# Performance work log

Measured on AMD Instinct MI355X. Metric: run time of the kernel, lower is better.

The kernel has to match this reference:

```python
import jax, jax.numpy as jnp
import numpy as np

# dims
B, P, H, W = 4, 512, 32, 32
C2 = P // 2            # 256 per-branch channels
HEAD = 4
DH = C2 // HEAD        # 64 head dim
L = H * W              # 1024 tokens
DI = 2 * C2            # 512 mamba d_inner (expand=2)
N = 64                 # d_state
R = (C2 + 15) // 16    # 16 dt_rank
KC = 4                 # d_conv


def setup_inputs() -> dict:
    key = jax.random.key(0)
    ks = jax.random.split(key, 32)
    f32 = jnp.float32
    def nrm(k, shape, s=0.02):
        return jax.random.normal(k, shape, f32) * s
    inp = {}
    inp['x'] = jax.random.normal(ks[0], (B, P, H, W), f32)
    # GambaCell rel-pos + gate conv
    inp['rel_h_c'] = jax.random.normal(ks[1], (1, C2, 1, H), f32)
    inp['rel_w_c'] = jax.random.normal(ks[2], (1, C2, W, 1), f32)
    inp['gate_w'] = nrm(ks[3], (C2, C2, 3))
    inp['gate_b'] = jnp.zeros((C2,), f32)
    # Mamba params
    inp['W_in'] = nrm(ks[4], (2 * DI, C2))
    inp['conv_w'] = nrm(ks[5], (DI, KC), 0.2)
    inp['conv_b'] = jnp.zeros((DI,), f32)
    inp['W_x'] = nrm(ks[6], (R + 2 * N, DI))
    inp['W_dt'] = nrm(ks[7], (DI, R), 0.1)
    inp['b_dt'] = jnp.full((DI,), -4.0, f32)
    inp['A_log'] = jnp.broadcast_to(jnp.log(jnp.arange(1, N + 1, dtype=f32)), (DI, N)).copy()
    inp['D_p'] = jnp.ones((DI,), f32)
    inp['W_out'] = nrm(ks[8], (C2, DI))
    # MHSA params (1x1 convs -> dense)
    inp['Wq'] = nrm(ks[9], (C2, C2)); inp['bq'] = jnp.zeros((C2,), f32)
    inp['Wk'] = nrm(ks[10], (C2, C2)); inp['bk'] = jnp.zeros((C2,), f32)
    inp['Wv'] = nrm(ks[11], (C2, C2)); inp['bv'] = jnp.zeros((C2,), f32)
    inp['rel_h_m'] = jax.random.normal(ks[12], (1, HEAD, DH, 1, H), f32) * 0.02
    inp['rel_w_m'] = jax.random.normal(ks[13], (1, HEAD, DH, W, 1), f32) * 0.02
    inp['reg_qk'] = jax.random.normal(ks[14], (1, L, L), f32)
    inp['reg_v'] = jax.random.normal(ks[15], (1, DH, L), f32)
    # Gating params
    inp['Wa'] = nrm(ks[16], (P, C2)); inp['ba'] = jnp.zeros((P,), f32)
    inp['Wb'] = nrm(ks[17], (P, C2)); inp['bb'] = jnp.zeros((P,), f32)
    inp['Wg'] = nrm(ks[18], (1, P)); inp['bg'] = jnp.zeros((1,), f32)
    return inp


def _silu(t):
    return t * jax.nn.sigmoid(t)


def _conv1x1(w, b, t):  # Conv2d kernel_size=1
    return jnp.einsum('oc,bchw->bohw', w, t) + b[None, :, None, None]


def _mamba(seq, W_in, conv_w, conv_b, W_x, W_dt, b_dt, A_log, D_p, W_out):
    # seq: (B, L, C2)
    Bn = seq.shape[0]
    xz = seq @ W_in.T                       # (B,L,2*DI)
    xi, z = jnp.split(xz, 2, axis=-1)
    # causal depthwise conv1d, kernel 4, left-pad 3, trimmed to L
    xc = jnp.transpose(xi, (0, 2, 1))       # (B,DI,L)
    xp = jnp.pad(xc, ((0, 0), (0, 0), (KC - 1, 0)))
    conv = conv_b[None, :, None]
    for kk in range(KC):
        conv = conv + conv_w[None, :, kk, None] * xp[:, :, kk:kk + L]
    xs = _silu(conv).transpose(0, 2, 1)     # (B,L,DI)
    x_dbl = xs @ W_x.T                      # (B,L,R+2N)
    dt = jax.nn.softplus(x_dbl[..., :R] @ W_dt.T + b_dt)   # (B,L,DI)
    Bm = x_dbl[..., R:R + N]                # (B,L,N)
    Cm = x_dbl[..., R + N:]                 # (B,L,N)
    A = -jnp.exp(A_log)                     # (DI,N)

    def step(h, t):
        dt_t, B_t, C_t, u_t = t             # (B,DI),(B,N),(B,N),(B,DI)
        dA = jnp.exp(dt_t[..., None] * A)   # (B,DI,N)
        h = dA * h + (dt_t * u_t)[..., None] * B_t[:, None, :]
        y = jnp.sum(h * C_t[:, None, :], axis=-1)
        return h, y

    h0 = jnp.zeros((Bn, DI, N), seq.dtype)
    scan_in = (dt.transpose(1, 0, 2), Bm.transpose(1, 0, 2),
               Cm.transpose(1, 0, 2), xs.transpose(1, 0, 2))
    _, ys = jax.lax.scan(step, h0, scan_in)  # (L,B,DI)
    y = ys.transpose(1, 0, 2) + D_p * xs
    y = y * _silu(z)
    return y @ W_out.T                      # (B,L,C2)


def _forward(x, rel_h_c, rel_w_c, gate_w, gate_b, W_in, conv_w, conv_b, W_x,
             W_dt, b_dt, A_log, D_p, W_out, Wq, bq, Wk, bk, Wv, bv,
             rel_h_m, rel_w_m, reg_qk, reg_v, Wa, ba, Wb, bb, Wg, bg):
    Bn = x.shape[0]
    x1, x2 = x[:, :C2], x[:, C2:]
    # --- GambaCell branch ---
    seq = x1.reshape(Bn, C2, L).transpose(0, 2, 1)          # (B,L,C2)
    pos = (rel_h_c + rel_w_c).reshape(1, C2, L).transpose(0, 2, 1)
    seq = seq + pos
    sc = seq.transpose(0, 2, 1)                             # (B,C2,L)
    ctx = jax.nn.sigmoid(
        jax.lax.conv_general_dilated(sc, gate_w, (1,), [(1, 1)],
                                     dimension_numbers=('NCH', 'OIH', 'NCH'))
        + gate_b[None, :, None]).transpose(0, 2, 1)          # (B,L,C2)
    ym = _mamba(seq, W_in, conv_w, conv_b, W_x, W_dt, b_dt, A_log, D_p, W_out)
    # faithful to original: view (B,L,C)->(B,C,H,W) with no permute
    out1 = (ym * ctx).reshape(Bn, C2, H, W)
    # --- MHSA branch ---
    q = _conv1x1(Wq, bq, x2).reshape(Bn, HEAD, DH, L)
    k = _conv1x1(Wk, bk, x2).reshape(Bn, HEAD, DH, L)
    v = _conv1x1(Wv, bv, x2).reshape(Bn, HEAD, DH, L)
    cc = jnp.einsum('bhdi,bhdj->bhij', q, k)                # content-content
    posm = (rel_h_m + rel_w_m).reshape(HEAD, DH, L)
    cp = jnp.einsum('hdi,bhdj->bhij', posm, q)              # position^T @ q
    energy = cc + cp                                         # (B,HEAD,L,L)
    e = jnp.concatenate([energy, jnp.broadcast_to(reg_qk[None], (Bn, 1, L, L))], axis=1)
    vp = jnp.concatenate([v, jnp.broadcast_to(reg_v[None], (Bn, 1, DH, L))], axis=1)
    attn = jax.nn.softmax(e, axis=-1)
    out = jnp.einsum('bndj,bnij->bndi', vp, attn)           # v @ attn^T
    out2 = out[:, :HEAD].reshape(Bn, C2, H, W)
    # --- Gating fusion ---
    a_proj = _conv1x1(Wa, ba, out1)
    b_proj = _conv1x1(Wb, bb, out2)
    ga = jax.nn.sigmoid(_conv1x1(Wg, bg, a_proj))
    gb = jax.nn.sigmoid(_conv1x1(Wg, bg, b_proj))
    return ga * a_proj + gb * b_proj                        # (B,P,H,W)


def reference(x, rel_h_c, rel_w_c, gate_w, gate_b, W_in, conv_w, conv_b, W_x,
              W_dt, b_dt, A_log, D_p, W_out, Wq, bq, Wk, bk, Wv, bv,
              rel_h_m, rel_w_m, reg_qk, reg_v, Wa, ba, Wb, bb, Wg, bg):
    return _forward(x, rel_h_c, rel_w_c, gate_w, gate_b, W_in, conv_w, conv_b,
                    W_x, W_dt, b_dt, A_log, D_p, W_out, Wq, bq, Wk, bk, Wv, bv,
                    rel_h_m, rel_w_m, reg_qk, reg_v, Wa, ba, Wb, bb, Wg, bg)
```

## Files before the change

### kernel.cpp

```cpp
#include <hip/hip_runtime.h>
#include <math.h>

static constexpr int Bn = 4, Pp = 512, C2 = 256, HEAD = 4, DHd = 64;
static constexpr int Ll = 1024, DIi = 512, Nn = 64, Rr = 16, KCc = 4;
static constexpr int XDW = 192;

#define DEVI __device__ __forceinline__

DEVI float sigf(float x){ return 1.0f/(1.0f+__expf(-x)); }
DEVI float softplusf(float x){ return x > 20.f ? x : log1pf(__expf(x)); }

DEVI unsigned short bfh(float f){
  unsigned int u = __float_as_uint(f);
  return (unsigned short)((u + 0x7FFFu + ((u>>16)&1u)) >> 16);
}
DEVI float bff(unsigned short h){ return __uint_as_float(((unsigned int)h)<<16); }

typedef __attribute__((ext_vector_type(8))) short  bf8v;
typedef __attribute__((ext_vector_type(4))) float  f4v;
typedef __attribute__((ext_vector_type(8))) unsigned short u16x8;

__global__ void k_transpose(const float* __restrict__ x, const float* __restrict__ rh,
                            const float* __restrict__ rw, float* __restrict__ seq,
                            float* __restrict__ x2seq){
  __shared__ float t[32][33];
  int b = blockIdx.z, c0 = blockIdx.y*32, l0 = blockIdx.x*32;
  for (int i = threadIdx.y; i < 32; i += 8)
    t[i][threadIdx.x] = x[((size_t)(b*Pp + c0 + i)*Ll) + l0 + threadIdx.x];
  __syncthreads();
  for (int i = threadIdx.y; i < 32; i += 8){
    int l = l0 + i, c = c0 + threadIdx.x;
    float v = t[threadIdx.x][i];
    if (c < C2){
      float pos = rh[c*32 + (l & 31)] + rw[c*32 + (l >> 5)];
      seq[(size_t)(b*Ll + l)*C2 + c] = v + pos;
    } else {
      x2seq[(size_t)(b*Ll + l)*C2 + (c - C2)] = v;
    }
  }
}

__global__ void __launch_bounds__(256) k_mgemmb(
    const float* __restrict__ A, const float* __restrict__ B,
    float* __restrict__ C, const float* __restrict__ bias,
    int M, int N, int K, int lda, int ldb, int ldc,
    long sA1, long sA2, long sB1, long sB2, long sC1, long sC2, int act)
{
  __shared__ __align__(16) unsigned short Ah[64*40], Al[64*40], Bh[64*40], Bl[64*40];
  int z = blockIdx.z;
  const float* Ab = A + (size_t)((z>>2)*sA1 + (z&3)*sA2);
  const float* Bb = B + (size_t)((z>>2)*sB1 + (z&3)*sB2);
  float*       Cb = C + (size_t)((z>>2)*sC1 + (z&3)*sC2);
  int m0 = blockIdx.y*64, n0 = blockIdx.x*64;
  int t = threadIdx.x;
  int w = t >> 6, l = t & 63;
  int g = l >> 4, r = l & 15;
  int row0 = w*16;

  f4v acc[4];
  #pragma unroll
  for (int j=0;j<4;++j) acc[j] = (f4v){0.f,0.f,0.f,0.f};

  int sr = t >> 2;
  int sc = (t & 3) * 8;

  for (int k0 = 0; k0 < K; k0 += 32){
    {
      const float* src = Ab + (size_t)(m0+sr)*lda + k0 + sc;
      float4 v0 = *(const float4*)(src);
      float4 v1 = *(const float4*)(src+4);
      float f[8] = {v0.x,v0.y,v0.z,v0.w,v1.x,v1.y,v1.z,v1.w};
      u16x8 hv, lv;
      #pragma unroll
      for (int i=0;i<8;++i){
        unsigned short h = bfh(f[i]); hv[i] = h;
        lv[i] = bfh(f[i] - bff(h));
      }
      *(u16x8*)&Ah[sr*40+sc] = hv;
      *(u16x8*)&Al[sr*40+sc] = lv;
    }
    {
      const float* src = Bb + (size_t)(n0+sr)*ldb + k0 + sc;
      float4 v0 = *(const float4*)(src);
      float4 v1 = *(const float4*)(src+4);
      float f[8] = {v0.x,v0.y,v0.z,v0.w,v1.x,v1.y,v1.z,v1.w};
      u16x8 hv, lv;
      #pragma unroll
      for (int i=0;i<8;++i){
        unsigned short h = bfh(f[i]); hv[i] = h;
        lv[i] = bfh(f[i] - bff(h));
      }
      *(u16x8*)&Bh[sr*40+sc] = hv;
      *(u16x8*)&Bl[sr*40+sc] = lv;
    }
    __syncthreads();
    bf8v a_h = *(const bf8v*)&Ah[(row0+r)*40 + g*8];
    bf8v a_l = *(const bf8v*)&Al[(row0+r)*40 + g*8];
    #pragma unroll
    for (int j=0;j<4;++j){
      bf8v b_h = *(const bf8v*)&Bh[(j*16+r)*40 + g*8];
      bf8v b_l = *(const bf8v*)&Bl[(j*16+r)*40 + g*8];
      acc[j] = __builtin_amdgcn_mfma_f32_16x16x32_bf16(a_h, b_h, acc[j], 0, 0, 0);
      acc[j] = __builtin_amdgcn_mfma_f32_16x16x32_bf16(a_h, b_l, acc[j], 0, 0, 0);
      acc[j] = __builtin_amdgcn_mfma_f32_16x16x32_bf16(a_l, b_h, acc[j], 0, 0, 0);
    }
    __syncthreads();
  }
  #pragma unroll
  for (int j=0;j<4;++j){
    int n = n0 + j*16 + r;
    float bv = bias ? bias[n] : 0.f;
    #pragma unroll
    for (int q=0;q<4;++q){
      int m = m0 + row0 + g*4 + q;
      float v = acc[j][q] + bv;
      if (act == 1) v = sigf(v);
      Cb[(size_t)m*ldc + n] = v;
    }
  }
}

__global__ void __launch_bounds__(256) k_m128(
    const float* __restrict__ A, const float* __restrict__ B,
    float* __restrict__ C, const float* __restrict__ bias,
    int M, int N, int K, int lda, int ldb, int ldc,
    long sA1, long sA2, long sB1, long sB2, long sC1, long sC2, int act)
{
  __shared__ __align__(16) unsigned short Ah[128*40], Al[128*40], Bh[128*40], Bl[128*40];
  int z = blockIdx.z;
  const float* Ab = A + (size_t)((z>>2)*sA1 + (z&3)*sA2);
  const float* Bb = B + (size_t)((z>>2)*sB1 + (z&3)*sB2);
  float*       Cb = C + (size_t)((z>>2)*sC1 + (z&3)*sC2);
  int m0 = blockIdx.y*128, n0 = blockIdx.x*128;
  int t = threadIdx.x;
  int w = t >> 6, l = t & 63;
  int g = l >> 4, r = l & 15;
  int row0 = w*32;

  f4v acc[2][8];
  #pragma unroll
  for (int i=0;i<2;++i)
    #pragma unroll
    for (int j=0;j<8;++j) acc[i][j] = (f4v){0.f,0.f,0.f,0.f};

  int sr = t >> 1;
  int sc = (t & 1) * 16;

  for (int k0 = 0; k0 < K; k0 += 32){
    {
      const float* src = Ab + (size_t)(m0+sr)*lda + k0 + sc;
      float4 v0 = *(const float4*)(src);
      float4 v1 = *(const float4*)(src+4);
      float4 v2 = *(const float4*)(src+8);
      float4 v3 = *(const float4*)(src+12);
      float f[16] = {v0.x,v0.y,v0.z,v0.w,v1.x,v1.y,v1.z,v1.w,
                     v2.x,v2.y,v2.z,v2.w,v3.x,v3.y,v3.z,v3.w};
      u16x8 hv0, lv0, hv1, lv1;
      #pragma unroll
      for (int i=0;i<8;++i){
        unsigned short h = bfh(f[i]); hv0[i] = h;
        lv0[i] = bfh(f[i] - bff(h));
      }
      #pragma unroll
      for (int i=0;i<8;++i){
        unsigned short h = bfh(f[8+i]); hv1[i] = h;
        lv1[i] = bfh(f[8+i] - bff(h));
      }
      *(u16x8*)&Ah[sr*40+sc]   = hv0;  *(u16x8*)&Ah[sr*40+sc+8] = hv1;
      *(u16x8*)&Al[sr*40+sc]   = lv0;  *(u16x8*)&Al[sr*40+sc+8] = lv1;
    }
    {
      const float* src = Bb + (size_t)(n0+sr)*ldb + k0 + sc;
      float4 v0 = *(const float4*)(src);
      float4 v1 = *(const float4*)(src+4);
      float4 v2 = *(const float4*)(src+8);
      float4 v3 = *(const float4*)(src+12);
      float f[16] = {v0.x,v0.y,v0.z,v0.w,v1.x,v1.y,v1.z,v1.w,
                     v2.x,v2.y,v2.z,v2.w,v3.x,v3.y,v3.z,v3.w};
      u16x8 hv0, lv0, hv1, lv1;
      #pragma unroll
      for (int i=0;i<8;++i){
        unsigned short h = bfh(f[i]); hv0[i] = h;
        lv0[i] = bfh(f[i] - bff(h));
      }
      #pragma unroll
      for (int i=0;i<8;++i){
        unsigned short h = bfh(f[8+i]); hv1[i] = h;
        lv1[i] = bfh(f[8+i] - bff(h));
      }
      *(u16x8*)&Bh[sr*40+sc]   = hv0;  *(u16x8*)&Bh[sr*40+sc+8] = hv1;
      *(u16x8*)&Bl[sr*40+sc]   = lv0;  *(u16x8*)&Bl[sr*40+sc+8] = lv1;
    }
    __syncthreads();
    bf8v a_h0 = *(const bf8v*)&Ah[(row0+r)*40 + g*8];
    bf8v a_l0 = *(const bf8v*)&Al[(row0+r)*40 + g*8];
    bf8v a_h1 = *(const bf8v*)&Ah[(row0+16+r)*40 + g*8];
    bf8v a_l1 = *(const bf8v*)&Al[(row0+16+r)*40 + g*8];
    #pragma unroll
    for (int j=0;j<8;++j){
      bf8v b_h = *(const bf8v*)&Bh[(j*16+r)*40 + g*8];
      bf8v b_l = *(const bf8v*)&Bl[(j*16+r)*40 + g*8];
      acc[0][j] = __builtin_amdgcn_mfma_f32_16x16x32_bf16(a_h0, b_h, acc[0][j], 0, 0, 0);
      acc[0][j] = __builtin_amdgcn_mfma_f32_16x16x32_bf16(a_h0, b_l, acc[0][j], 0, 0, 0);
      acc[0][j] = __builtin_amdgcn_mfma_f32_16x16x32_bf16(a_l0, b_h, acc[0][j], 0, 0, 0);
      acc[1][j] = __builtin_amdgcn_mfma_f32_16x16x32_bf16(a_h1, b_h, acc[1][j], 0, 0, 0);
      acc[1][j] = __builtin_amdgcn_mfma_f32_16x16x32_bf16(a_h1, b_l, acc[1][j], 0, 0, 0);
      acc[1][j] = __builtin_amdgcn_mfma_f32_16x16x32_bf16(a_l1, b_h, acc[1][j], 0, 0, 0);
    }
    __syncthreads();
  }
  #pragma unroll
  for (int i=0;i<2;++i){
    #pragma unroll
    for (int j=0;j<8;++j){
      int n = n0 + j*16 + r;
      float bv = bias ? bias[n] : 0.f;
      #pragma unroll
      for (int q=0;q<4;++q){
        int m = m0 + row0 + i*16 + g*4 + q;
        float v = acc[i][j][q] + bv;
        if (act == 1) v = sigf(v);
        Cb[(size_t)m*ldc + n] = v;
      }
    }
  }
}

__global__ void k_padwx(const float* __restrict__ W_x, float* __restrict__ W_xp){
  int idx = blockIdx.x*256 + threadIdx.x;
  int row = idx >> 9;
  W_xp[idx] = (row < 144) ? W_x[(size_t)(row)*512 + (idx & 511)] : 0.f;
}

__global__ void k_im2col(const float* __restrict__ seq, float* __restrict__ A2){
  int idx = blockIdx.x*256 + threadIdx.x;
  int j  = idx % 768;
  int bl = idx / 768;
  int kk = j >> 8, c = j & 255;
  int l = bl & 1023, b = bl >> 10;
  int ls = l + kk - 1;
  float v = 0.f;
  if (ls >= 0 && ls < Ll) v = seq[(size_t)(b*Ll + ls)*C2 + c];
  A2[idx] = v;
}

__global__ void k_packw(const float* __restrict__ gw, float* __restrict__ W2){
  int idx = blockIdx.x*256 + threadIdx.x;
  int j = idx % 768, o = idx / 768;
  int kk = j >> 8, i = j & 255;
  W2[idx] = gw[(size_t)(o*256 + i)*3 + kk];
}

__global__ void k_dwconv(const float* __restrict__ xz, const float* __restrict__ cw,
                         const float* __restrict__ cb, float* __restrict__ xs){
  int idx = blockIdx.x*256 + threadIdx.x;
  int d = idx & 511; int bl = idx >> 9; int l = bl & 1023; int b = bl >> 10;
  float s = cb[d];
  #pragma unroll
  for (int kk = 0; kk < 4; ++kk){
    int ls = l - 3 + kk;
    if (ls >= 0) s = fmaf(cw[d*4+kk], xz[(size_t)(b*Ll+ls)*1024 + d], s);
  }
  xs[idx] = s * sigf(s);
}

__global__ void k_pret(const float* __restrict__ xdbl, const float* __restrict__ xs,
                       const float* __restrict__ W_dt, const float* __restrict__ b_dt,
                       float* __restrict__ dtT, float* __restrict__ dtuT){
  __shared__ float X[32][17];
  __shared__ float Wd[32][17];
  __shared__ float xsb[32][33];
  int b = blockIdx.z, d0 = blockIdx.y*32, l0 = blockIdx.x*32;
  int tx = threadIdx.x, ty = threadIdx.y;
  for (int i = ty; i < 32; i += 8){
    if (tx < 16)      X[i][tx]      = xdbl[(size_t)(b*Ll + l0 + i)*XDW + tx];
    else              Wd[i][tx-16]  = W_dt[(size_t)(d0 + i)*16 + tx - 16];
    xsb[i][tx] = xs[(size_t)(b*Ll + l0 + i)*512 + d0 + tx];
  }
  __syncthreads();
  for (int dy = ty; dy < 32; dy += 8){
    int d = d0 + dy;
    float v = b_dt[d];
    #pragma unroll
    for (int r = 0; r < 16; ++r) v = fmaf(Wd[dy][r], X[tx][r], v);
    float dt = softplusf(v);
    size_t o = ((size_t)(b*512 + d))*Ll + l0 + tx;
    dtT[o]  = dt;
    dtuT[o] = dt * xsb[tx][dy];
  }
}

__global__ void __launch_bounds__(256, 1) k_scan6(
    const float* __restrict__ dtT, const float* __restrict__ dtuT,
    const float* __restrict__ xdbl, const float* __restrict__ A_log,
    float* __restrict__ yT){
  __shared__ float Bs[32*64];
  __shared__ float Cs[32*64];
  __shared__ float pb[4*32*65];
  int t = threadIdx.x;
  int w = t >> 6, lane = t & 63;
  int blk = blockIdx.x;
  int b = blk >> 7, grp = blk & 127;
  int d = grp*4 + w;
  float Ac = -__expf(A_log[d*64 + lane]);
  float h = 0.f;
  size_t base = (size_t)b*Ll;
  size_t bd   = ((size_t)(b*512 + d))*Ll;
  int jl = lane & 31;
  bool lo = lane < 32;
  float* pbw = &pb[w*2080];
  for (int c0 = 0; c0 < Ll; c0 += 32){
    float dtv = 0.f, duv = 0.f;
    if (lo){
      dtv = dtT[bd + c0 + lane];
      duv = dtuT[bd + c0 + lane];
    }
    #pragma unroll
    for (int kk = 0; kk < 8; ++kk){
      int i = t + kk*256;
      int row = i >> 6, col = i & 63;
      size_t r2 = (base + c0 + row)*XDW;
      Bs[i] = xdbl[r2 + 16 + col];
      Cs[i] = xdbl[r2 + 80 + col];
    }
    __syncthreads();
    float ev[32], gv[32];
    #pragma unroll
    for (int l = 0; l < 32; ++l){
      float sdt = __shfl(dtv, l);
      float sdu = __shfl(duv, l);
      ev[l] = __expf(sdt*Ac);
      gv[l] = sdu*Bs[l*64 + lane];
    }
    #pragma unroll
    for (int l = 0; l < 32; ++l){
      h = fmaf(ev[l], h, gv[l]);
      pbw[l*65 + lane] = h*Cs[l*64 + lane];
    }
    __syncthreads();
    {
      const float* rp = &pbw[jl*65 + (lo ? 0 : 32)];
      float s0=0.f, s1=0.f, s2=0.f, s3=0.f;
      #pragma unroll
      for (int n = 0; n < 32; n += 4){
        s0 += rp[n]; s1 += rp[n+1]; s2 += rp[n+2]; s3 += rp[n+3];
      }
      float p = (s0+s1)+(s2+s3);
      p += __shfl_xor(p, 32);
      if (lo) yT[bd + c0 + jl] = p;
    }
    __syncthreads();
  }
}

__global__ void k_ytrans(const float* __restrict__ yT, const float* __restrict__ xs,
                         const float* __restrict__ xz, const float* __restrict__ D_p,
                         float* __restrict__ y){
  __shared__ float t[32][33];
  int b = blockIdx.z, d0 = blockIdx.y*32, l0 = blockIdx.x*32;
  int tx = threadIdx.x, ty = threadIdx.y;
  for (int i = ty; i < 32; i += 8)
    t[i][tx] = yT[((size_t)(b*512 + d0 + i))*Ll + l0 + tx];
  __syncthreads();
  for (int i = ty; i < 32; i += 8){
    int d = d0 + tx;
    size_t bl = (size_t)b*Ll + l0 + i;
    float p  = t[tx][i];
    float u  = xs[bl*512 + d];
    float zv = xz[bl*1024 + 512 + d];
    y[bl*512 + d] = (p + D_p[d]*u) * (zv * sigf(zv));
  }
}

__global__ void k_pack_ab(const float* __restrict__ qt, const float* __restrict__ kt,
                          const float* __restrict__ rhm, const float* __restrict__ rwm,
                          float* __restrict__ Ab, float* __restrict__ Bb){
  int idx = blockIdx.x*256 + threadIdx.x;
  int dd = idx & 127;
  int i  = (idx >> 7) & 1023;
  int h  = (idx >> 17) & 3;
  int b  = idx >> 19;
  float av, bv;
  if (dd < 64){
    size_t q = (size_t)(b*Ll + i)*C2 + h*64 + dd;
    av = qt[q]; bv = kt[q];
  } else {
    int d = dd - 64;
    av = rhm[(h*64+d)*32 + (i & 31)] + rwm[(h*64+d)*32 + (i >> 5)];
    bv = qt[(size_t)(b*Ll + i)*C2 + h*64 + d];
  }
  Ab[idx] = av; Bb[idx] = bv;
}

__global__ void k_vtrans(const float* __restrict__ vt, float* __restrict__ vT){
  __shared__ float t[32][33];
  int b = blockIdx.z, c0 = blockIdx.y*32, j0 = blockIdx.x*32;
  for (int i = threadIdx.y; i < 32; i += 8)
    t[i][threadIdx.x] = vt[(size_t)(b*Ll + j0 + i)*C2 + c0 + threadIdx.x];
  __syncthreads();
  for (int i = threadIdx.y; i < 32; i += 8)
    vT[((size_t)(b*C2 + c0 + i))*Ll + j0 + threadIdx.x] = t[threadIdx.x][i];
}

__global__ void __launch_bounds__(256) k_softmax(float* __restrict__ e){
  __shared__ float red[4];
  __shared__ float red2[4];
  size_t row = blockIdx.x;
  float* p = e + row*1024;
  int t = threadIdx.x;
  float v0 = p[t], v1 = p[t+256], v2 = p[t+512], v3 = p[t+768];
  float mx = fmaxf(fmaxf(v0,v1), fmaxf(v2,v3));
  #pragma unroll
  for (int off=32; off; off>>=1) mx = fmaxf(mx, __shfl_xor(mx, off));
  if ((t&63)==0) red[t>>6] = mx;
  __syncthreads();
  mx = fmaxf(fmaxf(red[0],red[1]), fmaxf(red[2],red[3]));
  v0 = __expf(v0-mx); v1 = __expf(v1-mx); v2 = __expf(v2-mx); v3 = __expf(v3-mx);
  float s = v0+v1+v2+v3;
  #pragma unroll
  for (int off=32; off; off>>=1) s += __shfl_xor(s, off);
  if ((t&63)==0) red2[t>>6] = s;
  __syncthreads();
  s = red2[0]+red2[1]+red2[2]+red2[3];
  float inv = 1.0f/s;
  p[t] = v0*inv; p[t+256] = v1*inv; p[t+512] = v2*inv; p[t+768] = v3*inv;
}

__global__ void k_mulshuf(const float* __restrict__ ym, const float* __restrict__ ctx,
                          float* __restrict__ out1t){
  __shared__ float t[32][33];
  int b = blockIdx.z >> 2, s1 = blockIdx.z & 3;
  int c0 = blockIdx.y*32, s00 = blockIdx.x*32;
  for (int i = threadIdx.y; i < 32; i += 8){
    int c = c0 + i;
    int l = c*4 + s1;
    size_t off = ((size_t)(b*Ll + l))*C2 + s00 + threadIdx.x;
    t[i][threadIdx.x] = ym[off] * ctx[off];
  }
  __syncthreads();
  for (int i = threadIdx.y; i < 32; i += 8){
    int s0 = s00 + i, c = c0 + threadIdx.x;
    int s = s1*256 + s0;
    out1t[((size_t)(b*Ll + s))*C2 + c] = t[threadIdx.x][i];
  }
}

__global__ void __launch_bounds__(256) k_gates(
    const float* __restrict__ ap, const float* __restrict__ bp,
    const float* __restrict__ Wg, const float* __restrict__ bg, float* __restrict__ g){
  __shared__ float ra[4], rb[4];
  int bl = blockIdx.x; int t = threadIdx.x;
  float sa = 0.f, sb = 0.f;
  const float* a = ap + (size_t)bl*512;
  const float* bq = bp + (size_t)bl*512;
  for (int pp = t; pp < 512; pp += 256){ float w = Wg[pp]; sa = fmaf(w, a[pp], sa); sb = fmaf(w, bq[pp], sb); }
  #pragma unroll
  for (int off=32; off; off>>=1){ sa += __shfl_xor(sa,off); sb += __shfl_xor(sb,off); }
  if ((t&63)==0){ ra[t>>6]=sa; rb[t>>6]=sb; }
  __syncthreads();
  if (t==0){
    float b0 = bg[0];
    g[bl]        = sigf(ra[0]+ra[1]+ra[2]+ra[3] + b0);
    g[4096 + bl] = sigf(rb[0]+rb[1]+rb[2]+rb[3] + b0);
  }
}

__global__ void k_final(const float* __restrict__ ap, const float* __restrict__ bp,
                        const float* __restrict__ g, float* __restrict__ out){
  int bpid = blockIdx.x; int b = bpid >> 9, p = bpid & 511;
  for (int l = threadIdx.x; l < Ll; l += 256){
    int bl = b*Ll + l;
    float ga = g[bl], gb = g[4096 + bl];
    out[((size_t)(b*Pp + p) << 10) + l] =
        ga*ap[(size_t)bl*512 + p] + gb*bp[(size_t)bl*512 + p];
  }
}

static inline void mgemm(hipStream_t s, const float* A, const float* B, float* C,
                         const float* bias, int M, int N, int K, int lda, int ldb, int ldc,
                         int act){
  dim3 g(N/64, M/64, 1), blk(256);
  k_mgemmb<<<g, blk, 0, s>>>(A,B,C,bias,M,N,K,lda,ldb,ldc, 0,0,0,0,0,0, act);
}

extern "C" void kernel_launch(void* const* d_in, const int* in_sizes, int n_in,
                              void* d_out, int out_size, void* d_ws, size_t ws_size,
                              hipStream_t stream) {
  const float* x      = (const float*)d_in[0];
  const float* rh_c   = (const float*)d_in[1];
  const float* rw_c   = (const float*)d_in[2];
  const float* gate_w = (const float*)d_in[3];
  const float* gate_b = (const float*)d_in[4];
  const float* W_in   = (const float*)d_in[5];
  const float* conv_w = (const float*)d_in[6];
  const float* conv_b = (const float*)d_in[7];
  const float* W_x    = (const float*)d_in[8];
  const float* W_dt   = (const float*)d_in[9];
  const float* b_dt   = (const float*)d_in[10];
  const float* A_log  = (const float*)d_in[11];
  const float* D_p    = (const float*)d_in[12];
  const float* W_out  = (const float*)d_in[13];
  const float* Wq     = (const float*)d_in[14];
  const float* bq     = (const float*)d_in[15];
  const float* Wk     = (const float*)d_in[16];
  const float* bk     = (const float*)d_in[17];
  const float* Wv     = (const float*)d_in[18];
  const float* bv     = (const float*)d_in[19];
  const float* rhm    = (const float*)d_in[20];
  const float* rwm    = (const float*)d_in[21];
  const float* Wa     = (const float*)d_in[24];
  const float* ba     = (const float*)d_in[25];
  const float* Wb     = (const float*)d_in[26];
  const float* bb     = (const float*)d_in[27];
  const float* Wg     = (const float*)d_in[28];
  const float* bg     = (const float*)d_in[29];
  float* out = (float*)d_out;
  float* ws  = (float*)d_ws;

  float* seq    = ws;
  float* x2seq  = ws +  1048576;
  float* qt     = ws +  2097152;
  float* kt     = ws +  3145728;
  float* vt     = ws +  4194304;
  float* Abuf   = ws +  5242880;
  float* Bbuf   = ws +  7340032;
  float* arena  = ws +  9437184;
  float* out2   = ws + 26214400;
  float* out1   = ws + 27262976;
  float* aproj  = ws + 28311552;
  float* bproj  = ws + 30408704;
  float* gates  = ws + 32505856;
  float* W2     = ws + 32514048;
  float* A2   = arena;
  float* ctx  = arena +  3145728;
  float* xz   = arena +  4194304;
  float* xs   = arena +  8388608;
  float* xdbl = arena + 10485760;
  float* yT   = arena + 11272192;
  float* yb   = arena + 13369344;
  float* ym   = arena + 15466496;
  float* energy = arena;
  float* vT   = aproj;
  float* dtT  = Abuf;
  float* dtuT = Bbuf;
  float* W_xp = qt;

  k_transpose<<<dim3(32,16,4), dim3(32,8), 0, stream>>>(x, rh_c, rw_c, seq, x2seq);

  mgemm(stream, x2seq, Wq, qt, bq, 4096,256,256, 256,256,256, 0);
  mgemm(stream, x2seq, Wk, kt, bk, 4096,256,256, 256,256,256, 0);
  mgemm(stream, x2seq, Wv, vt, bv, 4096,256,256, 256,256,256, 0);
  k_pack_ab<<<8192, 256, 0, stream>>>(qt, kt, rhm, rwm, Abuf, Bbuf);
  k_vtrans<<<dim3(32,8,4), dim3(32,8), 0, stream>>>(vt, vT);
  {
    dim3 g(8, 8, 16), blk(256);
    k_m128<<<g, blk, 0, stream>>>(Abuf, Bbuf, energy, nullptr,
        1024,1024,128, 128,128,1024,
        4L*131072, 131072, 4L*131072, 131072, 4L*1048576, 1048576, 0);
  }
  k_softmax<<<16384, 256, 0, stream>>>(energy);
  {
    dim3 g(1, 16, 16), blk(256);
    k_mgemmb<<<g, blk, 0, stream>>>(energy, vT, out2, nullptr,
        1024,64,1024, 1024,1024,256,
        4L*1048576, 1048576, 262144, 65536, 262144, 64, 0);
  }

  k_packw<<<768, 256, 0, stream>>>(gate_w, W2);
  k_padwx<<<384, 256, 0, stream>>>(W_x, W_xp);
  k_im2col<<<12288, 256, 0, stream>>>(seq, A2);
  mgemm(stream, A2, W2, ctx, gate_b, 4096,256,768, 768,768,256, 1);
  {
    dim3 g(8, 32, 1), blk(256);
    k_m128<<<g, blk, 0, stream>>>(seq, W_in, xz, nullptr,
        4096,1024,256, 256,256,1024, 0,0,0,0,0,0, 0);
  }
  k_dwconv<<<8192, 256, 0, stream>>>(xz, conv_w, conv_b, xs);
  mgemm(stream, xs, W_xp, xdbl, nullptr, 4096,192,512, 512,512,XDW, 0);
  k_pret<<<dim3(32,16,4), dim3(32,8), 0, stream>>>(xdbl, xs, W_dt, b_dt, dtT, dtuT);
  k_scan6<<<512, 256, 0, stream>>>(dtT, dtuT, xdbl, A_log, yT);
  k_ytrans<<<dim3(32,16,4), dim3(32,8), 0, stream>>>(yT, xs, xz, D_p, yb);
  mgemm(stream, yb, W_out, ym, nullptr, 4096,256,512, 512,512,256, 0);
  k_mulshuf<<<dim3(8,8,16), dim3(32,8), 0, stream>>>(ym, ctx, out1);

  mgemm(stream, out1, Wa, aproj, ba, 4096,512,256, 256,256,512, 0);
  mgemm(stream, out2, Wb, bproj, bb, 4096,512,256, 256,256,512, 0);
  k_gates<<<4096, 256, 0, stream>>>(aproj, bproj, Wg, bg, gates);
  k_final<<<2048, 256, 0, stream>>>(aproj, bproj, gates, out);
}
```

Measured before the change: 565.3 us.

## Pre-split GEMM operands into bf16 hi/lo planes in producer kernels

```diff
diff --git a/kernel.cpp b/kernel.cpp
--- a/kernel.cpp
+++ b/kernel.cpp
@@ -15,14 +15,26 @@
   return (unsigned short)((u + 0x7FFFu + ((u>>16)&1u)) >> 16);
 }
 DEVI float bff(unsigned short h){ return __uint_as_float(((unsigned int)h)<<16); }
+DEVI void wsplit(float v, unsigned short* __restrict__ h, unsigned short* __restrict__ l,
+                 size_t i){
+  unsigned short hh = bfh(v);
+  h[i] = hh; l[i] = bfh(v - bff(hh));
+}
 
 typedef __attribute__((ext_vector_type(8))) short  bf8v;
 typedef __attribute__((ext_vector_type(4))) float  f4v;
 typedef __attribute__((ext_vector_type(8))) unsigned short u16x8;
 
+__global__ void k_split(const float* __restrict__ src, unsigned short* __restrict__ h,
+                        unsigned short* __restrict__ l, int n){
+  int i = blockIdx.x*256 + threadIdx.x;
+  if (i < n) wsplit(src[i], h, l, i);
+}
+
 __global__ void k_transpose(const float* __restrict__ x, const float* __restrict__ rh,
                             const float* __restrict__ rw, float* __restrict__ seq,
-                            float* __restrict__ x2seq){
+                            unsigned short* __restrict__ sh, unsigned short* __restrict__ sl,
+                            unsigned short* __restrict__ x2h, unsigned short* __restrict__ x2l){
   __shared__ float t[32][33];
   int b = blockIdx.z, c0 = blockIdx.y*32, l0 = blockIdx.x*32;
   for (int i = threadIdx.y; i < 32; i += 8)
@@ -33,24 +45,31 @@
     float v = t[threadIdx.x][i];
     if (c < C2){
       float pos = rh[c*32 + (l & 31)] + rw[c*32 + (l >> 5)];
-      seq[(size_t)(b*Ll + l)*C2 + c] = v + pos;
+      float vv = v + pos;
+      size_t o = (size_t)(b*Ll + l)*C2 + c;
+      seq[o] = vv;
+      wsplit(vv, sh, sl, o);
     } else {
-      x2seq[(size_t)(b*Ll + l)*C2 + (c - C2)] = v;
-    }
-  }
-}
-
-__global__ void __launch_bounds__(256) k_mgemmb(
-    const float* __restrict__ A, const float* __restrict__ B,
+      size_t o = (size_t)(b*Ll + l)*C2 + (c - C2);
+      wsplit(v, x2h, x2l, o);
+    }
+  }
+}
+
+__global__ void __launch_bounds__(256) k_hgemm(
+    const unsigned short* __restrict__ Ahp, const unsigned short* __restrict__ Alp,
+    const unsigned short* __restrict__ Bhp, const unsigned short* __restrict__ Blp,
     float* __restrict__ C, const float* __restrict__ bias,
     int M, int N, int K, int lda, int ldb, int ldc,
     long sA1, long sA2, long sB1, long sB2, long sC1, long sC2, int act)
 {
   __shared__ __align__(16) unsigned short Ah[64*40], Al[64*40], Bh[64*40], Bl[64*40];
   int z = blockIdx.z;
-  const float* Ab = A + (size_t)((z>>2)*sA1 + (z&3)*sA2);
-  const float* Bb = B + (size_t)((z>>2)*sB1 + (z&3)*sB2);
-  float*       Cb = C + (size_t)((z>>2)*sC1 + (z&3)*sC2);
+  const unsigned short* Abh = Ahp + (size_t)((z>>2)*sA1 + (z&3)*sA2);
+  const unsigned short* Abl = Alp + (size_t)((z>>2)*sA1 + (z&3)*sA2);
+  const unsigned short* Bbh = Bhp + (size_t)((z>>2)*sB1 + (z&3)*sB2);
+  const unsigned short* Bbl = Blp + (size_t)((z>>2)*sB1 + (z&3)*sB2);
+  float* Cb = C + (size_t)((z>>2)*sC1 + (z&3)*sC2);
   int m0 = blockIdx.y*64, n0 = blockIdx.x*64;
   int t = threadIdx.x;
   int w = t >> 6, l = t & 63;
@@ -65,34 +84,12 @@
   int sc = (t & 3) * 8;
 
   for (int k0 = 0; k0 < K; k0 += 32){
-    {
-      const float* src = Ab + (size_t)(m0+sr)*lda + k0 + sc;
-      float4 v0 = *(const float4*)(src);
-      float4 v1 = *(const float4*)(src+4);
-      float f[8] = {v0.x,v0.y,v0.z,v0.w,v1.x,v1.y,v1.z,v1.w};
-      u16x8 hv, lv;
-      #pragma unroll
-      for (int i=0;i<8;++i){
-        unsigned short h = bfh(f[i]); hv[i] = h;
-        lv[i] = bfh(f[i] - bff(h));
-      }
-      *(u16x8*)&Ah[sr*40+sc] = hv;
-      *(u16x8*)&Al[sr*40+sc] = lv;
-    }
-    {
-      const float* src = Bb + (size_t)(n0+sr)*ldb + k0 + sc;
-      float4 v0 = *(const float4*)(src);
-      float4 v1 = *(const float4*)(src+4);
-      float f[8] = {v0.x,v0.y,v0.z,v0.w,v1.x,v1.y,v1.z,v1.w};
-      u16x8 hv, lv;
-      #pragma unroll
-      for (int i=0;i<8;++i){
-        unsigned short h = bfh(f[i]); hv[i] = h;
-        lv[i] = bfh(f[i] - bff(h));
-      }
-      *(u16x8*)&Bh[sr*40+sc] = hv;
-      *(u16x8*)&Bl[sr*40+sc] = lv;
-    }
+    size_t ao = (size_t)(m0+sr)*lda + k0 + sc;
+    size_t bo = (size_t)(n0+sr)*ldb + k0 + sc;
+    *(u16x8*)&Ah[sr*40+sc] = *(const u16x8*)&Abh[ao];
+    *(u16x8*)&Al[sr*40+sc] = *(const u16x8*)&Abl[ao];
+    *(u16x8*)&Bh[sr*40+sc] = *(const u16x8*)&Bbh[bo];
+    *(u16x8*)&Bl[sr*40+sc] = *(const u16x8*)&Bbl[bo];
     __syncthreads();
     bf8v a_h = *(const bf8v*)&Ah[(row0+r)*40 + g*8];
     bf8v a_l = *(const bf8v*)&Al[(row0+r)*40 + g*8];
@@ -120,17 +117,20 @@
   }
 }
 
-__global__ void __launch_bounds__(256) k_m128(
-    const float* __restrict__ A, const float* __restrict__ B,
+__global__ void __launch_bounds__(256) k_h128(
+    const unsigned short* __restrict__ Ahp, const unsigned short* __restrict__ Alp,
+    const unsigned short* __restrict__ Bhp, const unsigned short* __restrict__ Blp,
     float* __restrict__ C, const float* __restrict__ bias,
     int M, int N, int K, int lda, int ldb, int ldc,
     long sA1, long sA2, long sB1, long sB2, long sC1, long sC2, int act)
 {
   __shared__ __align__(16) unsigned short Ah[128*40], Al[128*40], Bh[128*40], Bl[128*40];
   int z = blockIdx.z;
-  const float* Ab = A + (size_t)((z>>2)*sA1 + (z&3)*sA2);
-  const float* Bb = B + (size_t)((z>>2)*sB1 + (z&3)*sB2);
-  float*       Cb = C + (size_t)((z>>2)*sC1 + (z&3)*sC2);
+  const unsigned short* Abh = Ahp + (size_t)((z>>2)*sA1 + (z&3)*sA2);
+  const unsigned short* Abl = Alp + (size_t)((z>>2)*sA1 + (z&3)*sA2);
+  const unsigned short* Bbh = Bhp + (size_t)((z>>2)*sB1 + (z&3)*sB2);
+  const unsigned short* Bbl = Blp + (size_t)((z>>2)*sB1 + (z&3)*sB2);
+  float* Cb = C + (size_t)((z>>2)*sC1 + (z&3)*sC2);
   int m0 = blockIdx.y*128, n0 = blockIdx.x*128;
   int t = threadIdx.x;
   int w = t >> 6, l = t & 63;
@@ -147,50 +147,16 @@
   int sc = (t & 1) * 16;
 
   for (int k0 = 0; k0 < K; k0 += 32){
-    {
-      const float* src = Ab + (size_t)(m0+sr)*lda + k0 + sc;
-      float4 v0 = *(const float4*)(src);
-      float4 v1 = *(const float4*)(src+4);
-      float4 v2 = *(const float4*)(src+8);
-      float4 v3 = *(const float4*)(src+12);
-      float f[16] = {v0.x,v0.y,v0.z,v0.w,v1.x,v1.y,v1.z,v1.w,
-                     v2.x,v2.y,v2.z,v2.w,v3.x,v3.y,v3.z,v3.w};
-      u16x8 hv0, lv0, hv1, lv1;
-      #pragma unroll
-      for (int i=0;i<8;++i){
-        unsigned short h = bfh(f[i]); hv0[i] = h;
-        lv0[i] = bfh(f[i] - bff(h));
-      }
-      #pragma unroll
-      for (int i=0;i<8;++i){
-        unsigned short h = bfh(f[8+i]); hv1[i] = h;
-        lv1[i] = bfh(f[8+i] - bff(h));
-      }
-      *(u16x8*)&Ah[sr*40+sc]   = hv0;  *(u16x8*)&Ah[sr*40+sc+8] = hv1;
-      *(u16x8*)&Al[sr*40+sc]   = lv0;  *(u16x8*)&Al[sr*40+sc+8] = lv1;
-    }
-    {
-      const float* src = Bb + (size_t)(n0+sr)*ldb + k0 + sc;
-      float4 v0 = *(const float4*)(src);
-      float4 v1 = *(const float4*)(src+4);
-      float4 v2 = *(const float4*)(src+8);
-      float4 v3 = *(const float4*)(src+12);
-      float f[16] = {v0.x,v0.y,v0.z,v0.w,v1.x,v1.y,v1.z,v1.w,
-                     v2.x,v2.y,v2.z,v2.w,v3.x,v3.y,v3.z,v3.w};
-      u16x8 hv0, lv0, hv1, lv1;
-      #pragma unroll
-      for (int i=0;i<8;++i){
-        unsigned short h = bfh(f[i]); hv0[i] = h;
-        lv0[i] = bfh(f[i] - bff(h));
-      }
-      #pragma unroll
-      for (int i=0;i<8;++i){
-        unsigned short h = bfh(f[8+i]); hv1[i] = h;
-        lv1[i] = bfh(f[8+i] - bff(h));
-      }
-      *(u16x8*)&Bh[sr*40+sc]   = hv0;  *(u16x8*)&Bh[sr*40+sc+8] = hv1;
-      *(u16x8*)&Bl[sr*40+sc]   = lv0;  *(u16x8*)&Bl[sr*40+sc+8] = lv1;
-    }
+    size_t ao = (size_t)(m0+sr)*lda + k0 + sc;
+    size_t bo = (size_t)(n0+sr)*ldb + k0 + sc;
+    *(u16x8*)&Ah[sr*40+sc]   = *(const u16x8*)&Abh[ao];
+    *(u16x8*)&Ah[sr*40+sc+8] = *(const u16x8*)&Abh[ao+8];
+    *(u16x8*)&Al[sr*40+sc]   = *(const u16x8*)&Abl[ao];
+    *(u16x8*)&Al[sr*40+sc+8] = *(const u16x8*)&Abl[ao+8];
+    *(u16x8*)&Bh[sr*40+sc]   = *(const u16x8*)&Bbh[bo];
+    *(u16x8*)&Bh[sr*40+sc+8] = *(const u16x8*)&Bbh[bo+8];
+    *(u16x8*)&Bl[sr*40+sc]   = *(const u16x8*)&Bbl[bo];
+    *(u16x8*)&Bl[sr*40+sc+8] = *(const u16x8*)&Bbl[bo+8];
     __syncthreads();
     bf8v a_h0 = *(const bf8v*)&Ah[(row0+r)*40 + g*8];
     bf8v a_l0 = *(const bf8v*)&Al[(row0+r)*40 + g*8];
@@ -226,42 +192,49 @@
   }
 }
 
-__global__ void k_padwx(const float* __restrict__ W_x, float* __restrict__ W_xp){
+__global__ void k_padwx(const float* __restrict__ W_x, unsigned short* __restrict__ h,
+                        unsigned short* __restrict__ l){
   int idx = blockIdx.x*256 + threadIdx.x;
   int row = idx >> 9;
-  W_xp[idx] = (row < 144) ? W_x[(size_t)(row)*512 + (idx & 511)] : 0.f;
-}
-
-__global__ void k_im2col(const float* __restrict__ seq, float* __restrict__ A2){
+  float v = (row < 144) ? W_x[(size_t)row*512 + (idx & 511)] : 0.f;
+  wsplit(v, h, l, idx);
+}
+
+__global__ void k_im2col(const float* __restrict__ seq, unsigned short* __restrict__ h,
+                         unsigned short* __restrict__ l){
   int idx = blockIdx.x*256 + threadIdx.x;
   int j  = idx % 768;
   int bl = idx / 768;
   int kk = j >> 8, c = j & 255;
-  int l = bl & 1023, b = bl >> 10;
-  int ls = l + kk - 1;
+  int ll = bl & 1023, b = bl >> 10;
+  int ls = ll + kk - 1;
   float v = 0.f;
   if (ls >= 0 && ls < Ll) v = seq[(size_t)(b*Ll + ls)*C2 + c];
-  A2[idx] = v;
-}
-
-__global__ void k_packw(const float* __restrict__ gw, float* __restrict__ W2){
+  wsplit(v, h, l, idx);
+}
+
+__global__ void k_packw(const float* __restrict__ gw, unsigned short* __restrict__ h,
+                        unsigned short* __restrict__ l){
   int idx = blockIdx.x*256 + threadIdx.x;
   int j = idx % 768, o = idx / 768;
   int kk = j >> 8, i = j & 255;
-  W2[idx] = gw[(size_t)(o*256 + i)*3 + kk];
+  wsplit(gw[(size_t)(o*256 + i)*3 + kk], h, l, idx);
 }
 
 __global__ void k_dwconv(const float* __restrict__ xz, const float* __restrict__ cw,
-                         const float* __restrict__ cb, float* __restrict__ xs){
+                         const float* __restrict__ cb, float* __restrict__ xs,
+                         unsigned short* __restrict__ h, unsigned short* __restrict__ l){
   int idx = blockIdx.x*256 + threadIdx.x;
-  int d = idx & 511; int bl = idx >> 9; int l = bl & 1023; int b = bl >> 10;
+  int d = idx & 511; int bl = idx >> 9; int ll = bl & 1023; int b = bl >> 10;
   float s = cb[d];
   #pragma unroll
   for (int kk = 0; kk < 4; ++kk){
-    int ls = l - 3 + kk;
+    int ls = ll - 3 + kk;
     if (ls >= 0) s = fmaf(cw[d*4+kk], xz[(size_t)(b*Ll+ls)*1024 + d], s);
   }
-  xs[idx] = s * sigf(s);
+  float v = s * sigf(s);
+  xs[idx] = v;
+  wsplit(v, h, l, idx);
 }
 
 __global__ void k_pret(const float* __restrict__ xdbl, const float* __restrict__ xs,
@@ -355,7 +328,7 @@
 
 __global__ void k_ytrans(const float* __restrict__ yT, const float* __restrict__ xs,
                          const float* __restrict__ xz, const float* __restrict__ D_p,
-                         float* __restrict__ y){
+                         unsigned short* __restrict__ h, unsigned short* __restrict__ l){
   __shared__ float t[32][33];
   int b = blockIdx.z, d0 = blockIdx.y*32, l0 = blockIdx.x*32;
   int tx = threadIdx.x, ty = threadIdx.y;
@@ -368,13 +341,15 @@
     float p  = t[tx][i];
     float u  = xs[bl*512 + d];
     float zv = xz[bl*1024 + 512 + d];
-    y[bl*512 + d] = (p + D_p[d]*u) * (zv * sigf(zv));
+    float v = (p + D_p[d]*u) * (zv * sigf(zv));
+    wsplit(v, h, l, bl*512 + d);
   }
 }
 
 __global__ void k_pack_ab(const float* __restrict__ qt, const float* __restrict__ kt,
                           const float* __restrict__ rhm, const float* __restrict__ rwm,
-                          float* __restrict__ Ab, float* __restrict__ Bb){
+                          unsigned short* __restrict__ Ahp, unsigned short* __restrict__ Alp,
+                          unsigned short* __restrict__ Bhp, unsigned short* __restrict__ Blp){
   int idx = blockIdx.x*256 + threadIdx.x;
   int dd = idx & 127;
   int i  = (idx >> 7) & 1023;
@@ -389,17 +364,21 @@
     av = rhm[(h*64+d)*32 + (i & 31)] + rwm[(h*64+d)*32 + (i >> 5)];
     bv = qt[(size_t)(b*Ll + i)*C2 + h*64 + d];
   }
-  Ab[idx] = av; Bb[idx] = bv;
-}
-
-__global__ void k_vtrans(const float* __restrict__ vt, float* __restrict__ vT){
+  wsplit(av, Ahp, Alp, idx);
+  wsplit(bv, Bhp, Blp, idx);
+}
+
+__global__ void k_vtrans(const float* __restrict__ vt, unsigned short* __restrict__ h,
+                         unsigned short* __restrict__ l){
   __shared__ float t[32][33];
   int b = blockIdx.z, c0 = blockIdx.y*32, j0 = blockIdx.x*32;
   for (int i = threadIdx.y; i < 32; i += 8)
     t[i][threadIdx.x] = vt[(size_t)(b*Ll + j0 + i)*C2 + c0 + threadIdx.x];
   __syncthreads();
-  for (int i = threadIdx.y; i < 32; i += 8)
-    vT[((size_t)(b*C2 + c0 + i))*Ll + j0 + threadIdx.x] = t[threadIdx.x][i];
+  for (int i = threadIdx.y; i < 32; i += 8){
+    size_t o = ((size_t)(b*C2 + c0 + i))*Ll + j0 + threadIdx.x;
+    wsplit(t[threadIdx.x][i], h, l, o);
+  }
 }
 
 __global__ void __launch_bounds__(256) k_softmax(float* __restrict__ e){
@@ -423,25 +402,31 @@
   __syncthreads();
   s = red2[0]+red2[1]+red2[2]+red2[3];
   float inv = 1.0f/s;
-  p[t] = v0*inv; p[t+256] = v1*inv; p[t+512] = v2*inv; p[t+768] = v3*inv;
+  unsigned short* ph = (unsigned short*)p;
+  float r0 = v0*inv, r1 = v1*inv, r2 = v2*inv, r3 = v3*inv;
+  unsigned short h0 = bfh(r0), h1 = bfh(r1), h2 = bfh(r2), h3 = bfh(r3);
+  ph[t]      = h0; ph[1024+t]      = bfh(r0 - bff(h0));
+  ph[t+256]  = h1; ph[1024+t+256]  = bfh(r1 - bff(h1));
+  ph[t+512]  = h2; ph[1024+t+512]  = bfh(r2 - bff(h2));
+  ph[t+768]  = h3; ph[1024+t+768]  = bfh(r3 - bff(h3));
 }
 
 __global__ void k_mulshuf(const float* __restrict__ ym, const float* __restrict__ ctx,
-                          float* __restrict__ out1t){
+                          unsigned short* __restrict__ h, unsigned short* __restrict__ l){
   __shared__ float t[32][33];
   int b = blockIdx.z >> 2, s1 = blockIdx.z & 3;
   int c0 = blockIdx.y*32, s00 = blockIdx.x*32;
   for (int i = threadIdx.y; i < 32; i += 8){
     int c = c0 + i;
-    int l = c*4 + s1;
-    size_t off = ((size_t)(b*Ll + l))*C2 + s00 + threadIdx.x;
+    int ll = c*4 + s1;
+    size_t off = ((size_t)(b*Ll + ll))*C2 + s00 + threadIdx.x;
     t[i][threadIdx.x] = ym[off] * ctx[off];
   }
   __syncthreads();
   for (int i = threadIdx.y; i < 32; i += 8){
     int s0 = s00 + i, c = c0 + threadIdx.x;
     int s = s1*256 + s0;
-    out1t[((size_t)(b*Ll + s))*C2 + c] = t[threadIdx.x][i];
+    wsplit(t[threadIdx.x][i], h, l, ((size_t)(b*Ll + s))*C2 + c);
   }
 }
 
@@ -476,11 +461,12 @@
   }
 }
 
-static inline void mgemm(hipStream_t s, const float* A, const float* B, float* C,
-                         const float* bias, int M, int N, int K, int lda, int ldb, int ldc,
-                         int act){
+typedef unsigned short us;
+static inline void hgemm(hipStream_t s, const us* Ah, const us* Al, const us* Bh, const us* Bl,
+                         float* C, const float* bias, int M, int N, int K,
+                         int lda, int ldb, int ldc, int act){
   dim3 g(N/64, M/64, 1), blk(256);
-  k_mgemmb<<<g, blk, 0, s>>>(A,B,C,bias,M,N,K,lda,ldb,ldc, 0,0,0,0,0,0, act);
+  k_hgemm<<<g, blk, 0, s>>>(Ah,Al,Bh,Bl,C,bias,M,N,K,lda,ldb,ldc, 0,0,0,0,0,0, act);
 }
 
 extern "C" void kernel_launch(void* const* d_in, const int* in_sizes, int n_in,
@@ -540,51 +526,79 @@
   float* yb   = arena + 13369344;
   float* ym   = arena + 15466496;
   float* energy = arena;
-  float* vT   = aproj;
-  float* dtT  = Abuf;
-  float* dtuT = Bbuf;
-  float* W_xp = qt;
-
-  k_transpose<<<dim3(32,16,4), dim3(32,8), 0, stream>>>(x, rh_c, rw_c, seq, x2seq);
-
-  mgemm(stream, x2seq, Wq, qt, bq, 4096,256,256, 256,256,256, 0);
-  mgemm(stream, x2seq, Wk, kt, bk, 4096,256,256, 256,256,256, 0);
-  mgemm(stream, x2seq, Wv, vt, bv, 4096,256,256, 256,256,256, 0);
-  k_pack_ab<<<8192, 256, 0, stream>>>(qt, kt, rhm, rwm, Abuf, Bbuf);
-  k_vtrans<<<dim3(32,8,4), dim3(32,8), 0, stream>>>(vt, vT);
+
+  us* seqh = (us*)out1;      us* seql = seqh + 1048576;
+  us* x2h  = (us*)x2seq;     us* x2l  = x2h + 1048576;
+  us* eAh  = (us*)Abuf;      us* eAl  = eAh + 2097152;
+  us* eBh  = (us*)Bbuf;      us* eBl  = eBh + 2097152;
+  us* vTh  = (us*)aproj;     us* vTl  = vTh + 1048576;
+  us* Wqh  = (us*)arena;     us* Wql  = Wqh + 65536;
+  us* Wkh  = Wqh + 131072;   us* Wkl  = Wqh + 196608;
+  us* Wvh  = Wqh + 262144;   us* Wvl  = Wqh + 327680;
+  us* Ph   = (us*)energy;    us* Pl   = Ph + 1024;
+  us* A2h  = (us*)A2;        us* A2l  = A2h + 3145728;
+  us* W2h  = (us*)W2;        us* W2l  = W2h + 196608;
+  us* Wm   = (us*)kt;
+  us* Winh = Wm;             us* Winl = Wm + 262144;
+  us* Woh  = Wm + 524288;    us* Wol  = Wm + 655360;
+  us* Wah  = Wm + 786432;    us* Wal  = Wm + 917504;
+  us* Wbh  = Wm + 1048576;   us* Wbl  = Wm + 1179648;
+  us* Wxh  = Wm + 1310720;   us* Wxl  = Wm + 1409024;
+  us* xsh  = (us*)qt;        us* xsl  = (us*)vt;
+  us* ybh  = (us*)yb;        us* ybl  = ybh + 2097152;
+  us* o1h  = (us*)out1;      us* o1l  = o1h + 1048576;
+  us* o2h  = (us*)qt;        us* o2l  = o2h + 1048576;
+  float* dtT  = Abuf;        float* dtuT = Bbuf;
+
+  k_transpose<<<dim3(32,16,4), dim3(32,8), 0, stream>>>(x, rh_c, rw_c, seq,
+                                                        seqh, seql, x2h, x2l);
+
+  k_split<<<256, 256, 0, stream>>>(Wq, Wqh, Wql, 65536);
+  k_split<<<256, 256, 0, stream>>>(Wk, Wkh, Wkl, 65536);
+  k_split<<<256, 256, 0, stream>>>(Wv, Wvh, Wvl, 65536);
+  hgemm(stream, x2h, x2l, Wqh, Wql, qt, bq, 4096,256,256, 256,256,256, 0);
+  hgemm(stream, x2h, x2l, Wkh, Wkl, kt, bk, 4096,256,256, 256,256,256, 0);
+  hgemm(stream, x2h, x2l, Wvh, Wvl, vt, bv, 4096,256,256, 256,256,256, 0);
+  k_pack_ab<<<8192, 256, 0, stream>>>(qt, kt, rhm, rwm, eAh, eAl, eBh, eBl);
+  k_vtrans<<<dim3(32,8,4), dim3(32,8), 0, stream>>>(vt, vTh, vTl);
   {
     dim3 g(8, 8, 16), blk(256);
-    k_m128<<<g, blk, 0, stream>>>(Abuf, Bbuf, energy, nullptr,
+    k_h128<<<g, blk, 0, stream>>>(eAh, eAl, eBh, eBl, energy, nullptr,
         1024,1024,128, 128,128,1024,
         4L*131072, 131072, 4L*131072, 131072, 4L*1048576, 1048576, 0);
   }
   k_softmax<<<16384, 256, 0, stream>>>(energy);
   {
     dim3 g(1, 16, 16), blk(256);
-    k_mgemmb<<<g, blk, 0, stream>>>(energy, vT, out2, nullptr,
-        1024,64,1024, 1024,1024,256,
-        4L*1048576, 1048576, 262144, 65536, 262144, 64, 0);
-  }
-
-  k_packw<<<768, 256, 0, stream>>>(gate_w, W2);
-  k_padwx<<<384, 256, 0, stream>>>(W_x, W_xp);
-  k_im2col<<<12288, 256, 0, stream>>>(seq, A2);
-  mgemm(stream, A2, W2, ctx, gate_b, 4096,256,768, 768,768,256, 1);
+    k_hgemm<<<g, blk, 0, stream>>>(Ph, Pl, vTh, vTl, out2, nullptr,
+        1024,64,1024, 2048,1024,256,
+        8388608, 2097152, 262144, 65536, 262144, 64, 0);
+  }
+
+  k_packw<<<768, 256, 0, stream>>>(gate_w, W2h, W2l);
+  k_padwx<<<384, 256, 0, stream>>>(W_x, Wxh, Wxl);
+  k_split<<<1024, 256, 0, stream>>>(W_in, Winh, Winl, 262144);
+  k_split<<<512, 256, 0, stream>>>(W_out, Woh, Wol, 131072);
+  k_split<<<512, 256, 0, stream>>>(Wa, Wah, Wal, 131072);
+  k_split<<<512, 256, 0, stream>>>(Wb, Wbh, Wbl, 131072);
+  k_im2col<<<12288, 256, 0, stream>>>(seq, A2h, A2l);
+  hgemm(stream, A2h, A2l, W2h, W2l, ctx, gate_b, 4096,256,768, 768,768,256, 1);
   {
     dim3 g(8, 32, 1), blk(256);
-    k_m128<<<g, blk, 0, stream>>>(seq, W_in, xz, nullptr,
+    k_h128<<<g, blk, 0, stream>>>(seqh, seql, Winh, Winl, xz, nullptr,
         4096,1024,256, 256,256,1024, 0,0,0,0,0,0, 0);
   }
-  k_dwconv<<<8192, 256, 0, stream>>>(xz, conv_w, conv_b, xs);
-  mgemm(stream, xs, W_xp, xdbl, nullptr, 4096,192,512, 512,512,XDW, 0);
+  k_dwconv<<<8192, 256, 0, stream>>>(xz, conv_w, conv_b, xs, xsh, xsl);
+  hgemm(stream, xsh, xsl, Wxh, Wxl, xdbl, nullptr, 4096,192,512, 512,512,XDW, 0);
   k_pret<<<dim3(32,16,4), dim3(32,8), 0, stream>>>(xdbl, xs, W_dt, b_dt, dtT, dtuT);
   k_scan6<<<512, 256, 0, stream>>>(dtT, dtuT, xdbl, A_log, yT);
-  k_ytrans<<<dim3(32,16,4), dim3(32,8), 0, stream>>>(yT, xs, xz, D_p, yb);
-  mgemm(stream, yb, W_out, ym, nullptr, 4096,256,512, 512,512,256, 0);
-  k_mulshuf<<<dim3(8,8,16), dim3(32,8), 0, stream>>>(ym, ctx, out1);
-
-  mgemm(stream, out1, Wa, aproj, ba, 4096,512,256, 256,256,512, 0);
-  mgemm(stream, out2, Wb, bproj, bb, 4096,512,256, 256,256,512, 0);
+  k_ytrans<<<dim3(32,16,4), dim3(32,8), 0, stream>>>(yT, xs, xz, D_p, ybh, ybl);
+  hgemm(stream, ybh, ybl, Woh, Wol, ym, nullptr, 4096,256,512, 512,512,256, 0);
+  k_mulshuf<<<dim3(8,8,16), dim3(32,8), 0, stream>>>(ym, ctx, o1h, o1l);
+
+  hgemm(stream, o1h, o1l, Wah, Wal, aproj, ba, 4096,512,256, 256,256,512, 0);
+  k_split<<<4096, 256, 0, stream>>>(out2, o2h, o2l, 1048576);
+  hgemm(stream, o2h, o2l, Wbh, Wbl, bproj, bb, 4096,512,256, 256,256,512, 0);
   k_gates<<<4096, 256, 0, stream>>>(aproj, bproj, Wg, bg, gates);
   k_final<<<2048, 256, 0, stream>>>(aproj, bproj, gates, out);
 }
```

Result: no change. 566.6 us (+0.2%).
